# Kernel optimization log

Measured on AMD Instinct MI355X. Metric: run time of the kernel, lower is better.

The kernel has to match this reference:

```python
import jax, jax.numpy as jnp
import numpy as np

EPS = 1e-05
MARGIN = 0.0


def setup_inputs() -> dict:
    key = jax.random.key(0)
    k1, k2 = jax.random.split(key)
    embeddings = jax.random.normal(k1, (512, 512), dtype=jnp.float32)
    labels = jax.random.randint(k2, (512,), 0, 32, dtype=jnp.int64)
    return {"embeddings": embeddings, "labels": labels}


def _pairwise_distance(e, squared=False):
    # e: [B, D] -> [B, B] euclidean distances
    dot = jnp.matmul(e, e.T)
    sq = jnp.diag(dot)
    d = sq[:, None] - 2.0 * dot + sq[None, :]
    d = jnp.maximum(d, 0.0)
    if not squared:
        zmask = (d == 0.0).astype(d.dtype)
        d = d + zmask * EPS
        d = jnp.sqrt(d) + EPS
        d = d * (1.0 - zmask)
    return d


def _triplet_mask(labels):
    B = labels.shape[0]
    not_eq = ~jnp.eye(B, dtype=bool)
    # distinct indices i != j, i != k, j != k  -> [B, B, B]
    distinct = not_eq[:, :, None] & not_eq[:, None, :] & not_eq[None, :, :]
    lab_eq = labels[None, :] == labels[:, None]  # symmetric [B, B]
    valid = lab_eq[:, :, None] & (~lab_eq[:, None, :])  # label[i]==label[j], label[i]!=label[k]
    return (distinct & valid).astype(jnp.float32)


def reference(embeddings, labels):
    d = _pairwise_distance(embeddings, squared=False)  # [B, B]
    # triplet_loss[a, p, n] = d[a, p] - d[a, n] + margin
    tl = d[:, :, None] - d[:, None, :] + MARGIN
    mask = _triplet_mask(labels)
    tl = jnp.maximum(mask * tl, 0.0)
    num_positive = jnp.sum((tl > 1e-05).astype(jnp.float32))
    num_valid = jnp.sum(mask)
    fraction_positive = num_positive / (num_valid + 1e-05)
    loss = jnp.sum(tl) / (num_positive + 1e-05)
    return (loss, fraction_positive)
```

## Files before the change

### kernel.cpp

```cpp
#include <hip/hip_runtime.h>

#define BSZ 512
#define EPSF 1e-5f
#define TILE 64
#define KT   32
#define NS   16
#define LDST 68

__device__ __forceinline__ float dist_xform(float v) {
    v = fmaxf(v, 0.0f);
    float z = (v == 0.0f) ? 1.0f : 0.0f;
    v = sqrtf(v + z * EPSF) + EPSF;
    return v * (1.0f - z);
}

__global__ __launch_bounds__(64) void dsq_kernel(const float* __restrict__ E,
                                                 float* __restrict__ P) {
    __shared__ float As[KT][LDST];
    __shared__ float Bs[KT][LDST];
    const int tid = threadIdx.x;
    const int tx = tid & 7, ty = tid >> 3;
    const int bj = blockIdx.x * TILE;
    const int bi = blockIdx.y * TILE;
    const int k0 = blockIdx.z * KT;

    const int lc  = (tid & 7) * 4;
    const int lr0 = tid >> 3;
#pragma unroll
    for (int p = 0; p < 8; ++p) {
        const int row = p * 8 + lr0;
        float4 av = *(const float4*)(E + (size_t)(bi + row) * BSZ + k0 + lc);
        float4 bv = *(const float4*)(E + (size_t)(bj + row) * BSZ + k0 + lc);
        As[lc  ][row] = av.x; As[lc+1][row] = av.y; As[lc+2][row] = av.z; As[lc+3][row] = av.w;
        Bs[lc  ][row] = bv.x; Bs[lc+1][row] = bv.y; Bs[lc+2][row] = bv.z; Bs[lc+3][row] = bv.w;
    }
    __syncthreads();

    float acc[8][8];
#pragma unroll
    for (int r = 0; r < 8; ++r)
#pragma unroll
        for (int c = 0; c < 8; ++c) acc[r][c] = 0.0f;

#pragma unroll 4
    for (int kk = 0; kk < KT; ++kk) {
        float4 A0 = *(const float4*)&As[kk][ty * 8];
        float4 A1 = *(const float4*)&As[kk][ty * 8 + 4];
        float4 B0 = *(const float4*)&Bs[kk][tx * 8];
        float4 B1 = *(const float4*)&Bs[kk][tx * 8 + 4];
        float ar[8] = {A0.x, A0.y, A0.z, A0.w, A1.x, A1.y, A1.z, A1.w};
        float br[8] = {B0.x, B0.y, B0.z, B0.w, B1.x, B1.y, B1.z, B1.w};
#pragma unroll
        for (int r = 0; r < 8; ++r)
#pragma unroll
            for (int c = 0; c < 8; ++c) {
                float d = ar[r] - br[c];
                acc[r][c] = fmaf(d, d, acc[r][c]);
            }
    }

    float* Pp = P + (size_t)blockIdx.z * BSZ * BSZ;
#pragma unroll
    for (int r = 0; r < 8; ++r) {
        float4 v0 = {acc[r][0], acc[r][1], acc[r][2], acc[r][3]};
        float4 v1 = {acc[r][4], acc[r][5], acc[r][6], acc[r][7]};
        float* dst = Pp + (size_t)(bi + ty * 8 + r) * BSZ + bj + tx * 8;
        *(float4*)dst       = v0;
        *(float4*)(dst + 4) = v1;
    }
}

__global__ __launch_bounds__(256) void triplet_kernel(const float* __restrict__ P,
                                                      const int* __restrict__ labels,
                                                      float* __restrict__ partial) {
    const int a = blockIdx.x;
    const int tid = threadIdx.x;
    __shared__ float drow[BSZ];
    __shared__ int   lab[BSZ];
    __shared__ int   poslist[BSZ];
    __shared__ int   npos_s;
    __shared__ float wsum[4];
    __shared__ int   wcnt[4];

    if (tid == 0) npos_s = 0;
    for (int t = tid; t < BSZ; t += 256) lab[t] = labels[t];

    if (tid < 128) {
        float4 s4 = {0.f, 0.f, 0.f, 0.f};
#pragma unroll
        for (int s = 0; s < NS; ++s) {
            float4 v = *(const float4*)(P + ((size_t)s * BSZ + a) * BSZ + tid * 4);
            s4.x += v.x; s4.y += v.y; s4.z += v.z; s4.w += v.w;
        }
        drow[tid * 4 + 0] = dist_xform(s4.x);
        drow[tid * 4 + 1] = dist_xform(s4.y);
        drow[tid * 4 + 2] = dist_xform(s4.z);
        drow[tid * 4 + 3] = dist_xform(s4.w);
    }
    __syncthreads();

    const int la = lab[a];
    for (int t = tid; t < BSZ; t += 256) {
        if (lab[t] == la && t != a) {
            int idx = atomicAdd(&npos_s, 1);
            poslist[idx] = t;
        }
    }
    __syncthreads();

    const int npos = npos_s;
    const int nneg = BSZ - 1 - npos;
    float sum = 0.0f;
    int   cnt = 0;
    const int total = npos * BSZ;
    for (int idx = tid; idx < total; idx += 256) {
        const int p = poslist[idx >> 9];
        const int n = idx & (BSZ - 1);
        if (lab[n] != la) {
            const float v = drow[p] - drow[n];
            if (v > 0.0f)  sum += v;
            if (v > 1e-5f) cnt++;
        }
    }
#pragma unroll
    for (int off = 32; off > 0; off >>= 1) {
        sum += __shfl_down(sum, off);
        cnt += __shfl_down(cnt, off);
    }
    const int wave = tid >> 6, lane = tid & 63;
    if (lane == 0) { wsum[wave] = sum; wcnt[wave] = cnt; }
    __syncthreads();
    if (tid == 0) {
        partial[a]           = wsum[0] + wsum[1] + wsum[2] + wsum[3];
        partial[BSZ + a]     = (float)(wcnt[0] + wcnt[1] + wcnt[2] + wcnt[3]);
        partial[2*BSZ + a]   = (float)npos * (float)nneg;
    }
}

__global__ __launch_bounds__(256) void final_kernel(const float* __restrict__ partial,
                                                    float* __restrict__ out) {
    const int tid = threadIdx.x;
    float s = partial[tid]         + partial[tid + 256];
    float c = partial[BSZ + tid]   + partial[BSZ + tid + 256];
    float v = partial[2*BSZ + tid] + partial[2*BSZ + tid + 256];
#pragma unroll
    for (int off = 32; off > 0; off >>= 1) {
        s += __shfl_down(s, off);
        c += __shfl_down(c, off);
        v += __shfl_down(v, off);
    }
    __shared__ float ws[4], wc[4], wv[4];
    const int wave = tid >> 6, lane = tid & 63;
    if (lane == 0) { ws[wave] = s; wc[wave] = c; wv[wave] = v; }
    __syncthreads();
    if (tid == 0) {
        float S = ws[0] + ws[1] + ws[2] + ws[3];
        float C = wc[0] + wc[1] + wc[2] + wc[3];
        float V = wv[0] + wv[1] + wv[2] + wv[3];
        out[0] = S / (C + 1e-5f);
        out[1] = C / (V + 1e-5f);
    }
}

extern "C" void kernel_launch(void* const* d_in, const int* in_sizes, int n_in,
                              void* d_out, int out_size, void* d_ws, size_t ws_size,
                              hipStream_t stream) {
    const float* E      = (const float*)d_in[0];
    const int*   labels = (const int*)d_in[1];
    float* out = (float*)d_out;

    float* P       = (float*)d_ws;
    float* partial = P + (size_t)NS * BSZ * BSZ;

    dsq_kernel<<<dim3(8, 8, NS), 64, 0, stream>>>(E, P);
    triplet_kernel<<<BSZ, 256, 0, stream>>>(P, labels, partial);
    final_kernel<<<1, 256, 0, stream>>>(partial, out);
}
```

Measured before the change: 86.16 us.

## Fuse final reduction into triplet kernel and enlarge distance tile blocks

The final reduction kernel is removed. The last triplet block to finish, found through an atomic counter that dsq_kernel resets, now computes the loss and fraction. Separately, the distance kernel goes from 64-thread blocks on 64x64 tiles to 256-thread blocks on 128x64 tiles, with 8x4 outputs per thread. This saves a kernel launch and raises occupancy per block, at the cost of atomics, thread fences and a reset that depends on launch ordering.

```diff
diff --git a/kernel.cpp b/kernel.cpp
--- a/kernel.cpp
+++ b/kernel.cpp
@@ -2,10 +2,15 @@
 
 #define BSZ 512
 #define EPSF 1e-5f
-#define TILE 64
 #define KT   32
 #define NS   16
-#define LDST 68
+#define TR   128
+#define TC   64
+#define ASTR 132
+#define BSTR 68
+
+#define WS_PARTIAL 8
+#define WS_P       2048
 
 __device__ __forceinline__ float dist_xform(float v) {
     v = fmaxf(v, 0.0f);
@@ -14,65 +19,72 @@
     return v * (1.0f - z);
 }
 
-__global__ __launch_bounds__(64) void dsq_kernel(const float* __restrict__ E,
-                                                 float* __restrict__ P) {
-    __shared__ float As[KT][LDST];
-    __shared__ float Bs[KT][LDST];
+__global__ __launch_bounds__(256) void dsq_kernel(const float* __restrict__ E,
+                                                  float* __restrict__ ws) {
+    if (blockIdx.x == 0 && blockIdx.y == 0 && blockIdx.z == 0 && threadIdx.x == 0) {
+        ((int*)ws)[3] = 0;
+    }
+
+    __shared__ __align__(16) float As[KT][ASTR];
+    __shared__ __align__(16) float Bs[KT][BSTR];
     const int tid = threadIdx.x;
-    const int tx = tid & 7, ty = tid >> 3;
-    const int bj = blockIdx.x * TILE;
-    const int bi = blockIdx.y * TILE;
+    const int tx = tid & 15;
+    const int ty = tid >> 4;
+    const int bi = blockIdx.x * TR;
+    const int bj = blockIdx.y * TC;
     const int k0 = blockIdx.z * KT;
 
-    const int lc  = (tid & 7) * 4;
-    const int lr0 = tid >> 3;
+    {
+        const int r0 = tid >> 3;
+        const int kc = (tid & 7) * 4;
 #pragma unroll
-    for (int p = 0; p < 8; ++p) {
-        const int row = p * 8 + lr0;
-        float4 av = *(const float4*)(E + (size_t)(bi + row) * BSZ + k0 + lc);
-        float4 bv = *(const float4*)(E + (size_t)(bj + row) * BSZ + k0 + lc);
-        As[lc  ][row] = av.x; As[lc+1][row] = av.y; As[lc+2][row] = av.z; As[lc+3][row] = av.w;
-        Bs[lc  ][row] = bv.x; Bs[lc+1][row] = bv.y; Bs[lc+2][row] = bv.z; Bs[lc+3][row] = bv.w;
+        for (int p = 0; p < 4; ++p) {
+            const int row = p * 32 + r0;
+            float4 v = *(const float4*)(E + (size_t)(bi + row) * BSZ + k0 + kc);
+            As[kc  ][row] = v.x; As[kc+1][row] = v.y; As[kc+2][row] = v.z; As[kc+3][row] = v.w;
+        }
+#pragma unroll
+        for (int p = 0; p < 2; ++p) {
+            const int row = p * 32 + r0;
+            float4 v = *(const float4*)(E + (size_t)(bj + row) * BSZ + k0 + kc);
+            Bs[kc  ][row] = v.x; Bs[kc+1][row] = v.y; Bs[kc+2][row] = v.z; Bs[kc+3][row] = v.w;
+        }
     }
     __syncthreads();
 
-    float acc[8][8];
+    float acc[8][4];
 #pragma unroll
     for (int r = 0; r < 8; ++r)
 #pragma unroll
-        for (int c = 0; c < 8; ++c) acc[r][c] = 0.0f;
+        for (int c = 0; c < 4; ++c) acc[r][c] = 0.0f;
 
 #pragma unroll 4
     for (int kk = 0; kk < KT; ++kk) {
         float4 A0 = *(const float4*)&As[kk][ty * 8];
         float4 A1 = *(const float4*)&As[kk][ty * 8 + 4];
-        float4 B0 = *(const float4*)&Bs[kk][tx * 8];
-        float4 B1 = *(const float4*)&Bs[kk][tx * 8 + 4];
+        float4 B0 = *(const float4*)&Bs[kk][tx * 4];
         float ar[8] = {A0.x, A0.y, A0.z, A0.w, A1.x, A1.y, A1.z, A1.w};
-        float br[8] = {B0.x, B0.y, B0.z, B0.w, B1.x, B1.y, B1.z, B1.w};
+        float br[4] = {B0.x, B0.y, B0.z, B0.w};
 #pragma unroll
         for (int r = 0; r < 8; ++r)
 #pragma unroll
-            for (int c = 0; c < 8; ++c) {
+            for (int c = 0; c < 4; ++c) {
                 float d = ar[r] - br[c];
                 acc[r][c] = fmaf(d, d, acc[r][c]);
             }
     }
 
-    float* Pp = P + (size_t)blockIdx.z * BSZ * BSZ;
+    float* Pp = ws + WS_P + (size_t)blockIdx.z * BSZ * BSZ;
 #pragma unroll
     for (int r = 0; r < 8; ++r) {
-        float4 v0 = {acc[r][0], acc[r][1], acc[r][2], acc[r][3]};
-        float4 v1 = {acc[r][4], acc[r][5], acc[r][6], acc[r][7]};
-        float* dst = Pp + (size_t)(bi + ty * 8 + r) * BSZ + bj + tx * 8;
-        *(float4*)dst       = v0;
-        *(float4*)(dst + 4) = v1;
+        float4 v = {acc[r][0], acc[r][1], acc[r][2], acc[r][3]};
+        *(float4*)(Pp + (size_t)(bi + ty * 8 + r) * BSZ + bj + tx * 4) = v;
     }
 }
 
-__global__ __launch_bounds__(256) void triplet_kernel(const float* __restrict__ P,
-                                                      const int* __restrict__ labels,
-                                                      float* __restrict__ partial) {
+__global__ __launch_bounds__(256) void triplet_kernel(const int* __restrict__ labels,
+                                                      float* __restrict__ ws,
+                                                      float* __restrict__ out) {
     const int a = blockIdx.x;
     const int tid = threadIdx.x;
     __shared__ float drow[BSZ];
@@ -81,10 +93,12 @@
     __shared__ int   npos_s;
     __shared__ float wsum[4];
     __shared__ int   wcnt[4];
+    __shared__ int   is_last;
 
     if (tid == 0) npos_s = 0;
     for (int t = tid; t < BSZ; t += 256) lab[t] = labels[t];
 
+    const float* P = ws + WS_P;
     if (tid < 128) {
         float4 s4 = {0.f, 0.f, 0.f, 0.f};
 #pragma unroll
@@ -130,35 +144,38 @@
     const int wave = tid >> 6, lane = tid & 63;
     if (lane == 0) { wsum[wave] = sum; wcnt[wave] = cnt; }
     __syncthreads();
+
+    float* partial = ws + WS_PARTIAL;
     if (tid == 0) {
         partial[a]           = wsum[0] + wsum[1] + wsum[2] + wsum[3];
         partial[BSZ + a]     = (float)(wcnt[0] + wcnt[1] + wcnt[2] + wcnt[3]);
         partial[2*BSZ + a]   = (float)npos * (float)nneg;
+        __threadfence();
+        int old = atomicAdd((int*)ws + 3, 1);
+        is_last = (old == BSZ - 1) ? 1 : 0;
     }
-}
+    __syncthreads();
 
-__global__ __launch_bounds__(256) void final_kernel(const float* __restrict__ partial,
-                                                    float* __restrict__ out) {
-    const int tid = threadIdx.x;
-    float s = partial[tid]         + partial[tid + 256];
-    float c = partial[BSZ + tid]   + partial[BSZ + tid + 256];
-    float v = partial[2*BSZ + tid] + partial[2*BSZ + tid + 256];
+    if (is_last) {
+        __threadfence();
+        float s = partial[tid]         + partial[tid + 256];
+        float c = partial[BSZ + tid]   + partial[BSZ + tid + 256];
+        float v = partial[2*BSZ + tid] + partial[2*BSZ + tid + 256];
 #pragma unroll
-    for (int off = 32; off > 0; off >>= 1) {
-        s += __shfl_down(s, off);
-        c += __shfl_down(c, off);
-        v += __shfl_down(v, off);
-    }
-    __shared__ float ws[4], wc[4], wv[4];
-    const int wave = tid >> 6, lane = tid & 63;
-    if (lane == 0) { ws[wave] = s; wc[wave] = c; wv[wave] = v; }
-    __syncthreads();
-    if (tid == 0) {
-        float S = ws[0] + ws[1] + ws[2] + ws[3];
-        float C = wc[0] + wc[1] + wc[2] + wc[3];
-        float V = wv[0] + wv[1] + wv[2] + wv[3];
-        out[0] = S / (C + 1e-5f);
-        out[1] = C / (V + 1e-5f);
+        for (int off = 32; off > 0; off >>= 1) {
+            s += __shfl_down(s, off);
+            c += __shfl_down(c, off);
+            v += __shfl_down(v, off);
+        }
+        if (lane == 0) { wsum[wave] = s; wcnt[wave] = (int)c; drow[wave] = v; }
+        __syncthreads();
+        if (tid == 0) {
+            float S = wsum[0] + wsum[1] + wsum[2] + wsum[3];
+            float C = (float)(wcnt[0] + wcnt[1] + wcnt[2] + wcnt[3]);
+            float V = drow[0] + drow[1] + drow[2] + drow[3];
+            out[0] = S / (C + 1e-5f);
+            out[1] = C / (V + 1e-5f);
+        }
     }
 }
 
@@ -168,11 +185,8 @@
     const float* E      = (const float*)d_in[0];
     const int*   labels = (const int*)d_in[1];
     float* out = (float*)d_out;
+    float* ws  = (float*)d_ws;
 
-    float* P       = (float*)d_ws;
-    float* partial = P + (size_t)NS * BSZ * BSZ;
-
-    dsq_kernel<<<dim3(8, 8, NS), 64, 0, stream>>>(E, P);
-    triplet_kernel<<<BSZ, 256, 0, stream>>>(P, labels, partial);
-    final_kernel<<<1, 256, 0, stream>>>(partial, out);
+    dsq_kernel<<<dim3(4, 8, NS), 256, 0, stream>>>(E, ws);
+    triplet_kernel<<<BSZ, 256, 0, stream>>>(labels, ws, out);
 }
```

Result: no change. 87.75 us (+1.8%).
